# Kernel optimization log

Hardware: AMD Instinct MI355X
Metric: run time of the kernel (lower is better)

Reference implementation:

```python
import jax, jax.numpy as jnp
import numpy as np

D_MODEL = 1024
N_HEAD = 16


def setup_inputs() -> dict:
    key = jax.random.key(0)
    ks = jax.random.split(key, 11)
    B, S, D = 2, 2048, D_MODEL
    scale = 1.0 / np.sqrt(D)
    inp = {
        "q": jax.random.normal(ks[0], (B, S, D), jnp.float32),
        "k": jax.random.normal(ks[1], (B, S, D), jnp.float32),
        "v": jax.random.normal(ks[2], (B, S, D), jnp.float32),
        "w_q": jax.random.normal(ks[3], (D, D), jnp.float32) * scale,
        "b_q": jnp.zeros((D,), jnp.float32),
        "w_k": jax.random.normal(ks[4], (D, D), jnp.float32) * scale,
        "b_k": jnp.zeros((D,), jnp.float32),
        "w_v": jax.random.normal(ks[5], (D, D), jnp.float32) * scale,
        "b_v": jnp.zeros((D,), jnp.float32),
        "w_o": jax.random.normal(ks[6], (D, D), jnp.float32) * scale,
        "b_o": jnp.zeros((D,), jnp.float32),
    }
    return inp


def _split_heads(x, n_head):
    # [B, S, D] -> [B, H, S, Dh]
    B, S, D = x.shape
    return x.reshape(B, S, n_head, D // n_head).transpose(0, 2, 1, 3)


def reference(q, k, v, w_q, b_q, w_k, b_k, w_v, b_v, w_o, b_o):
    # torch Linear: y = x @ W.T + b
    qp = q @ w_q.T + b_q
    kp = k @ w_k.T + b_k
    vp = v @ w_v.T + b_v
    qh = _split_heads(qp, N_HEAD)  # [B,H,S,Dh]
    kh = _split_heads(kp, N_HEAD)
    vh = _split_heads(vp, N_HEAD)
    d_head = qh.shape[-1]
    score = jnp.einsum("bhsd,bhtd->bhst", qh, kh) / jnp.sqrt(jnp.float32(d_head))
    attn = jax.nn.softmax(score, axis=-1)
    out = jnp.einsum("bhst,bhtd->bhsd", attn, vh)  # [B,H,S,Dh]
    B, H, S, Dh = out.shape
    out = out.transpose(0, 2, 1, 3).reshape(B, S, H * Dh)  # concat heads
    return out @ w_o.T + b_o
```

## Files before the change

### kernel.cpp

```cpp
#include <hip/hip_runtime.h>

typedef __bf16 bf16_t;
typedef __bf16 bf16x8 __attribute__((ext_vector_type(8)));
typedef __bf16 bf16x4 __attribute__((ext_vector_type(4)));
typedef float f32x4 __attribute__((ext_vector_type(4)));

#define MFMA16(a, b, c) __builtin_amdgcn_mfma_f32_16x16x32_bf16((a), (b), (c), 0, 0, 0)

#define GLOAD_LDS16(gsrc, ldst)                                                     \
  __builtin_amdgcn_global_load_lds(                                                 \
      (const __attribute__((address_space(1))) void*)(gsrc),                        \
      (__attribute__((address_space(3))) void*)(ldst), 16, 0, 0)

__global__ __launch_bounds__(256) void cast_all(
    const float* __restrict__ s0, const float* __restrict__ s1, const float* __restrict__ s2,
    const float* __restrict__ s3, const float* __restrict__ s4, const float* __restrict__ s5,
    const float* __restrict__ s6,
    bf16_t* __restrict__ d0, bf16_t* __restrict__ d1, bf16_t* __restrict__ d2,
    bf16_t* __restrict__ d3, bf16_t* __restrict__ d4, bf16_t* __restrict__ d5,
    bf16_t* __restrict__ d6) {
  const int a = blockIdx.y;
  const float* s = a == 0 ? s0 : a == 1 ? s1 : a == 2 ? s2 : a == 3 ? s3
                 : a == 4 ? s4 : a == 5 ? s5 : s6;
  bf16_t* d = a == 0 ? d0 : a == 1 ? d1 : a == 2 ? d2 : a == 3 ? d3
            : a == 4 ? d4 : a == 5 ? d5 : d6;
  const int n = a < 3 ? (2 * 2048 * 1024) : (1024 * 1024);
  int i = (blockIdx.x * 256 + threadIdx.x) * 4;
  if (i >= n) return;
  float4 v = *reinterpret_cast<const float4*>(s + i);
  bf16x4 o;
  o[0] = (bf16_t)v.x; o[1] = (bf16_t)v.y; o[2] = (bf16_t)v.z; o[3] = (bf16_t)v.w;
  *reinterpret_cast<bf16x4*>(d + i) = o;
}

template <int OUTF32>
__device__ __forceinline__ void gemm_core(
    const bf16_t* __restrict__ A, const bf16_t* __restrict__ B,
    const float* __restrict__ bias, void* __restrict__ Cout,
    int bm, int bn, float scalep, bf16_t* __restrict__ As, bf16_t* __restrict__ Bs) {
  const int tid = threadIdx.x, lane = tid & 63, wid = tid >> 6;
  const int wr = wid >> 1, wc = wid & 1;
  const int l15 = lane & 15, g = lane >> 4, l7 = l15 & 7;
  const int sr = lane >> 3;
  const int sg = (lane & 7) ^ sr;
  f32x4 acc[4][2] = {};

  const bf16_t* Arow = A + (size_t)(bm + wid * 32 + sr) * 1024 + sg * 8;
  const bf16_t* Brow = B + (size_t)(bn + wid * 16 + sr) * 1024 + sg * 8;

  auto stage = [&](int t, int buf) {
    const int k0 = t * 64;
    bf16_t* Ad = As + buf * 8192 + wid * 2048;
    bf16_t* Bd = Bs + buf * 4096 + wid * 1024;
#pragma unroll
    for (int a = 0; a < 4; a++)
      GLOAD_LDS16(Arow + (size_t)a * 8 * 1024 + k0, Ad + a * 512);
#pragma unroll
    for (int bI = 0; bI < 2; bI++)
      GLOAD_LDS16(Brow + (size_t)bI * 8 * 1024 + k0, Bd + bI * 512);
  };

  stage(0, 0);
  __syncthreads();
  for (int t = 0; t < 16; t++) {
    if (t < 15) stage(t + 1, (t + 1) & 1);
    const bf16_t* Ab = As + (t & 1) * 8192;
    const bf16_t* Bb = Bs + (t & 1) * 4096;
#pragma unroll
    for (int kk = 0; kk < 2; kk++) {
      const int gsw = ((kk * 4 + g) ^ l7) * 8;
      bf16x8 af[4], bfr[2];
#pragma unroll
      for (int mi = 0; mi < 4; mi++)
        af[mi] = *reinterpret_cast<const bf16x8*>(&Ab[(wr * 64 + mi * 16 + l15) * 64 + gsw]);
#pragma unroll
      for (int ni = 0; ni < 2; ni++)
        bfr[ni] = *reinterpret_cast<const bf16x8*>(&Bb[(wc * 32 + ni * 16 + l15) * 64 + gsw]);
      __builtin_amdgcn_s_setprio(1);
#pragma unroll
      for (int mi = 0; mi < 4; mi++)
#pragma unroll
        for (int ni = 0; ni < 2; ni++)
          acc[mi][ni] = MFMA16(af[mi], bfr[ni], acc[mi][ni]);
      __builtin_amdgcn_s_setprio(0);
    }
    __syncthreads();
  }

#pragma unroll
  for (int mi = 0; mi < 4; mi++)
#pragma unroll
    for (int ni = 0; ni < 2; ni++) {
      const int row = bm + wr * 64 + mi * 16 + g * 4;
      const int col = bn + wc * 32 + ni * 16 + l15;
      const float bv = bias[col];
#pragma unroll
      for (int r = 0; r < 4; r++) {
        float v = (acc[mi][ni][r] + bv) * scalep;
        if (OUTF32)
          reinterpret_cast<float*>(Cout)[(size_t)(row + r) * 1024 + col] = v;
        else
          reinterpret_cast<bf16_t*>(Cout)[(size_t)(row + r) * 1024 + col] = (bf16_t)v;
      }
    }
}

__global__ __launch_bounds__(256) void qkv_gemm(
    const bf16_t* __restrict__ qb, const bf16_t* __restrict__ kb, const bf16_t* __restrict__ vb,
    const bf16_t* __restrict__ wqb, const bf16_t* __restrict__ wkb, const bf16_t* __restrict__ wvb,
    const float* __restrict__ bq, const float* __restrict__ bk, const float* __restrict__ bv,
    bf16_t* __restrict__ QP, bf16_t* __restrict__ KP, bf16_t* __restrict__ VP, float qscale) {
  __shared__ bf16_t As[2 * 128 * 64];
  __shared__ bf16_t Bs[2 * 64 * 64];
  const int id = blockIdx.x;
  const int sw = (id & 7) * 192 + (id >> 3);
  const int z = sw >> 9, rem = sw & 511;
  const int by = rem >> 4, bx = rem & 15;
  const bf16_t* A = z == 0 ? qb : z == 1 ? kb : vb;
  const bf16_t* B = z == 0 ? wqb : z == 1 ? wkb : wvb;
  const float* bias = z == 0 ? bq : z == 1 ? bk : bv;
  bf16_t* C = z == 0 ? QP : z == 1 ? KP : VP;
  gemm_core<0>(A, B, bias, C, by * 128, bx * 64, z == 0 ? qscale : 1.0f, As, Bs);
}

__global__ __launch_bounds__(256) void out_gemm(
    const bf16_t* __restrict__ A, const bf16_t* __restrict__ B,
    const float* __restrict__ bias, float* __restrict__ C) {
  __shared__ bf16_t As[2 * 128 * 64];
  __shared__ bf16_t Bs[2 * 64 * 64];
  const int id = blockIdx.x;
  const int sw = (id & 7) * 64 + (id >> 3);
  const int by = sw >> 4, bx = sw & 15;
  gemm_core<1>(A, B, bias, C, by * 128, bx * 64, 1.0f, As, Bs);
}

__global__ __launch_bounds__(256) void transpose_v64(
    const bf16_t* __restrict__ VP, bf16_t* __restrict__ VT) {
  __shared__ bf16_t t[64][72];
  const int tid = threadIdx.x;
  const int bh = blockIdx.y, b = bh >> 4, h = bh & 15;
  const int sbase = blockIdx.x * 64;
#pragma unroll
  for (int i = 0; i < 2; i++) {
    int c = tid + i * 256;
    int r = c >> 3, cc = (c & 7) * 8;
    *reinterpret_cast<bf16x8*>(&t[r][cc]) =
        *reinterpret_cast<const bf16x8*>(&VP[(size_t)(b * 2048 + sbase + r) * 1024 + h * 64 + cc]);
  }
  __syncthreads();
#pragma unroll
  for (int i = 0; i < 2; i++) {
    int c = tid + i * 256;
    int d = c >> 3, scc = (c & 7) * 8;
    bf16x8 v;
#pragma unroll
    for (int j = 0; j < 8; j++) v[j] = t[scc + j][d];
    *reinterpret_cast<bf16x8*>(&VT[(size_t)(bh * 64 + d) * 2048 + sbase + scc]) = v;
  }
}

__global__ __launch_bounds__(512) void attn_fwd(
    const bf16_t* __restrict__ Q, const bf16_t* __restrict__ K,
    const bf16_t* __restrict__ VT, bf16_t* __restrict__ O) {
  __shared__ bf16_t Kl[2 * 64 * 64];
  __shared__ bf16_t Vl[2 * 64 * 64];
  __shared__ bf16_t Pl[8][16 * 64];
  const int tid = threadIdx.x, lane = tid & 63, wid = tid >> 6;
  const int l15 = lane & 15, g = lane >> 4, l7 = l15 & 7;
  const int id = blockIdx.x;
  const int sw = (id & 7) * 64 + (id >> 3);
  const int bh = sw >> 4, qblk = sw & 15;
  const int b = bh >> 4, h = bh & 15;
  const int qbase = qblk * 128;

  const int qrow = b * 2048 + qbase + wid * 16 + l15;
  const bf16x8 qf0 = *reinterpret_cast<const bf16x8*>(&Q[(size_t)qrow * 1024 + h * 64 + g * 8]);
  const bf16x8 qf1 = *reinterpret_cast<const bf16x8*>(&Q[(size_t)qrow * 1024 + h * 64 + 32 + g * 8]);

  const int sr = lane >> 3, sg = (lane & 7) ^ sr;
  const bf16_t* Ksrc = K + (size_t)(b * 2048 + wid * 8 + sr) * 1024 + h * 64 + sg * 8;
  const bf16_t* Vsrc = VT + (size_t)(bh * 64 + wid * 8 + sr) * 2048 + sg * 8;

  float ssum = 0.0f;
  f32x4 oacc[4] = {};

  auto stage = [&](int kt, int buf) {
    GLOAD_LDS16(Ksrc + (size_t)kt * 1024, Kl + buf * 4096 + wid * 512);
    GLOAD_LDS16(Vsrc + kt, Vl + buf * 4096 + wid * 512);
  };

  stage(0, 0);
  __syncthreads();
  for (int t = 0; t < 32; t++) {
    if (t < 31) stage((t + 1) * 64, (t + 1) & 1);
    const bf16_t* Kb = Kl + (t & 1) * 4096;
    const bf16_t* Vb = Vl + (t & 1) * 4096;

    f32x4 sacc[4] = {};
    __builtin_amdgcn_s_setprio(1);
#pragma unroll
    for (int ni = 0; ni < 4; ni++) {
      const int krow = (ni * 16 + l15) * 64;
      bf16x8 kf0 = *reinterpret_cast<const bf16x8*>(&Kb[krow + ((g ^ l7) * 8)]);
      bf16x8 kf1 = *reinterpret_cast<const bf16x8*>(&Kb[krow + (((4 + g) ^ l7) * 8)]);
      sacc[ni] = MFMA16(kf0, qf0, sacc[ni]);
      sacc[ni] = MFMA16(kf1, qf1, sacc[ni]);
    }
    __builtin_amdgcn_s_setprio(0);

    float rs = 0.0f;
#pragma unroll
    for (int ni = 0; ni < 4; ni++)
#pragma unroll
      for (int r = 0; r < 4; r++) {
        float e = exp2f(sacc[ni][r]);
        sacc[ni][r] = e;
        rs += e;
      }
    rs += __shfl_xor(rs, 16);
    rs += __shfl_xor(rs, 32);
    ssum += rs;

#pragma unroll
    for (int ni = 0; ni < 4; ni++) {
      bf16x4 pv;
#pragma unroll
      for (int r = 0; r < 4; r++) pv[r] = (bf16_t)sacc[ni][r];
      *reinterpret_cast<bf16x4*>(
          &Pl[wid][l15 * 64 + (((2 * ni + (g >> 1)) ^ l7) * 8) + (g & 1) * 4]) = pv;
    }

    __builtin_amdgcn_s_setprio(1);
#pragma unroll
    for (int c = 0; c < 2; c++) {
      const int gp = ((c * 4 + g) ^ l7) * 8;
      bf16x8 pf = *reinterpret_cast<const bf16x8*>(&Pl[wid][l15 * 64 + gp]);
#pragma unroll
      for (int dn = 0; dn < 4; dn++) {
        bf16x8 vf = *reinterpret_cast<const bf16x8*>(&Vb[(dn * 16 + l15) * 64 + gp]);
        oacc[dn] = MFMA16(pf, vf, oacc[dn]);
      }
    }
    __builtin_amdgcn_s_setprio(0);
    __syncthreads();
  }

  float si[4];
#pragma unroll
  for (int r = 0; r < 4; r++) si[r] = 1.0f / __shfl(ssum, g * 4 + r);
  const int orow = b * 2048 + qbase + wid * 16 + g * 4;
#pragma unroll
  for (int dn = 0; dn < 4; dn++)
#pragma unroll
    for (int r = 0; r < 4; r++)
      O[(size_t)(orow + r) * 1024 + h * 64 + dn * 16 + l15] = (bf16_t)(oacc[dn][r] * si[r]);
}

extern "C" void kernel_launch(void* const* d_in, const int* in_sizes, int n_in,
                              void* d_out, int out_size, void* d_ws, size_t ws_size,
                              hipStream_t stream) {
  const float* q  = (const float*)d_in[0];
  const float* k  = (const float*)d_in[1];
  const float* v  = (const float*)d_in[2];
  const float* wq = (const float*)d_in[3];
  const float* bq = (const float*)d_in[4];
  const float* wk = (const float*)d_in[5];
  const float* bk = (const float*)d_in[6];
  const float* wv = (const float*)d_in[7];
  const float* bv = (const float*)d_in[8];
  const float* wo = (const float*)d_in[9];
  const float* bo = (const float*)d_in[10];

  char* ws = (char*)d_ws;
  const size_t MB = 1024 * 1024;
  bf16_t* qb  = (bf16_t*)(ws + 0 * MB);
  bf16_t* kb  = (bf16_t*)(ws + 8 * MB);
  bf16_t* vb  = (bf16_t*)(ws + 16 * MB);
  bf16_t* QP  = (bf16_t*)(ws + 24 * MB);
  bf16_t* KP  = (bf16_t*)(ws + 32 * MB);
  bf16_t* VP  = (bf16_t*)(ws + 40 * MB);
  bf16_t* wqb = (bf16_t*)(ws + 48 * MB);
  bf16_t* wkb = (bf16_t*)(ws + 50 * MB);
  bf16_t* wvb = (bf16_t*)(ws + 52 * MB);
  bf16_t* wob = (bf16_t*)(ws + 54 * MB);
  bf16_t* VTb = (bf16_t*)(ws + 8 * MB);
  bf16_t* AO  = (bf16_t*)(ws + 0 * MB);

  const float QSCALE = 0.125f * 1.44269504089f;

  cast_all<<<dim3(4096, 7), 256, 0, stream>>>(q, k, v, wq, wk, wv, wo,
                                              qb, kb, vb, wqb, wkb, wvb, wob);
  qkv_gemm<<<1536, 256, 0, stream>>>(qb, kb, vb, wqb, wkb, wvb, bq, bk, bv,
                                     QP, KP, VP, QSCALE);
  transpose_v64<<<dim3(32, 32), 256, 0, stream>>>(VP, VTb);
  attn_fwd<<<512, 512, 0, stream>>>(QP, KP, VTb, AO);
  out_gemm<<<512, 256, 0, stream>>>(AO, wob, bo, (float*)d_out);
}
```

Baseline: 237.8 us.

## Triple-buffer GEMM K-loop with explicit vmcnt waits, retile QKV, shrink attention blocks

```diff
diff --git a/kernel.cpp b/kernel.cpp
--- a/kernel.cpp
+++ b/kernel.cpp
@@ -33,66 +33,73 @@
   *reinterpret_cast<bf16x4*>(d + i) = o;
 }
 
-template <int OUTF32>
-__device__ __forceinline__ void gemm_core(
+template <int OUTF32, int NFRAG>
+__device__ __forceinline__ void gemm_core3(
     const bf16_t* __restrict__ A, const bf16_t* __restrict__ B,
     const float* __restrict__ bias, void* __restrict__ Cout,
     int bm, int bn, float scalep, bf16_t* __restrict__ As, bf16_t* __restrict__ Bs) {
   const int tid = threadIdx.x, lane = tid & 63, wid = tid >> 6;
   const int wr = wid >> 1, wc = wid & 1;
-  const int l15 = lane & 15, g = lane >> 4, l7 = l15 & 7;
-  const int sr = lane >> 3;
-  const int sg = (lane & 7) ^ sr;
-  f32x4 acc[4][2] = {};
-
-  const bf16_t* Arow = A + (size_t)(bm + wid * 32 + sr) * 1024 + sg * 8;
-  const bf16_t* Brow = B + (size_t)(bn + wid * 16 + sr) * 1024 + sg * 8;
-
-  auto stage = [&](int t, int buf) {
-    const int k0 = t * 64;
-    bf16_t* Ad = As + buf * 8192 + wid * 2048;
-    bf16_t* Bd = Bs + buf * 4096 + wid * 1024;
-#pragma unroll
-    for (int a = 0; a < 4; a++)
-      GLOAD_LDS16(Arow + (size_t)a * 8 * 1024 + k0, Ad + a * 512);
-#pragma unroll
-    for (int bI = 0; bI < 2; bI++)
-      GLOAD_LDS16(Brow + (size_t)bI * 8 * 1024 + k0, Bd + bI * 512);
+  const int l15 = lane & 15, g = lane >> 4;
+  f32x4 acc[4][NFRAG] = {};
+
+  constexpr int ABUF = 4096;
+  constexpr int BBUF = NFRAG * 1024;
+
+  const int arow = wid * 16 + (lane >> 2);
+  const int sc = (lane & 3) * 8;
+  const bf16_t* Ap0 = A + (size_t)(bm + arow) * 1024 + sc;
+  const bf16_t* Ap1 = Ap0 + (size_t)64 * 1024;
+  const bf16_t* Bp0 = B + (size_t)(bn + arow) * 1024 + sc;
+  const bf16_t* Bp1 = Bp0 + (size_t)64 * 1024;
+
+  auto stage = [&](int k0, int buf) {
+    bf16_t* Ad = As + buf * ABUF;
+    bf16_t* Bd = Bs + buf * BBUF;
+    GLOAD_LDS16(Ap0 + k0, Ad + wid * 512);
+    GLOAD_LDS16(Ap1 + k0, Ad + 2048 + wid * 512);
+    GLOAD_LDS16(Bp0 + k0, Bd + wid * 512);
+    if constexpr (NFRAG == 4) GLOAD_LDS16(Bp1 + k0, Bd + 2048 + wid * 512);
   };
 
   stage(0, 0);
-  __syncthreads();
-  for (int t = 0; t < 16; t++) {
-    if (t < 15) stage(t + 1, (t + 1) & 1);
-    const bf16_t* Ab = As + (t & 1) * 8192;
-    const bf16_t* Bb = Bs + (t & 1) * 4096;
-#pragma unroll
-    for (int kk = 0; kk < 2; kk++) {
-      const int gsw = ((kk * 4 + g) ^ l7) * 8;
-      bf16x8 af[4], bfr[2];
-#pragma unroll
-      for (int mi = 0; mi < 4; mi++)
-        af[mi] = *reinterpret_cast<const bf16x8*>(&Ab[(wr * 64 + mi * 16 + l15) * 64 + gsw]);
-#pragma unroll
-      for (int ni = 0; ni < 2; ni++)
-        bfr[ni] = *reinterpret_cast<const bf16x8*>(&Bb[(wc * 32 + ni * 16 + l15) * 64 + gsw]);
-      __builtin_amdgcn_s_setprio(1);
-#pragma unroll
-      for (int mi = 0; mi < 4; mi++)
-#pragma unroll
-        for (int ni = 0; ni < 2; ni++)
-          acc[mi][ni] = MFMA16(af[mi], bfr[ni], acc[mi][ni]);
-      __builtin_amdgcn_s_setprio(0);
-    }
-    __syncthreads();
+  stage(32, 1);
+  for (int t = 0; t < 32; t++) {
+    const int kn = (t < 30) ? (t + 2) * 32 : 0;
+    stage(kn, (t + 2) % 3);
+    if constexpr (NFRAG == 4)
+      asm volatile("s_waitcnt vmcnt(8)" ::: "memory");
+    else
+      asm volatile("s_waitcnt vmcnt(6)" ::: "memory");
+    __builtin_amdgcn_s_barrier();
+    __builtin_amdgcn_sched_barrier(0);
+    const bf16_t* Ab = As + (t % 3) * ABUF;
+    const bf16_t* Bb = Bs + (t % 3) * BBUF;
+    bf16x8 af[4], bfr[NFRAG];
+#pragma unroll
+    for (int mi = 0; mi < 4; mi++)
+      af[mi] = *reinterpret_cast<const bf16x8*>(&Ab[(wr * 64 + mi * 16 + l15) * 32 + g * 8]);
+#pragma unroll
+    for (int ni = 0; ni < NFRAG; ni++)
+      bfr[ni] = *reinterpret_cast<const bf16x8*>(
+          &Bb[(wc * (NFRAG * 16) + ni * 16 + l15) * 32 + g * 8]);
+    __builtin_amdgcn_s_setprio(1);
+#pragma unroll
+    for (int mi = 0; mi < 4; mi++)
+#pragma unroll
+      for (int ni = 0; ni < NFRAG; ni++)
+        acc[mi][ni] = MFMA16(af[mi], bfr[ni], acc[mi][ni]);
+    __builtin_amdgcn_s_setprio(0);
+    __builtin_amdgcn_sched_barrier(0);
+    __builtin_amdgcn_s_barrier();
   }
 
 #pragma unroll
   for (int mi = 0; mi < 4; mi++)
 #pragma unroll
-    for (int ni = 0; ni < 2; ni++) {
+    for (int ni = 0; ni < NFRAG; ni++) {
       const int row = bm + wr * 64 + mi * 16 + g * 4;
-      const int col = bn + wc * 32 + ni * 16 + l15;
+      const int col = bn + wc * (NFRAG * 16) + ni * 16 + l15;
       const float bv = bias[col];
 #pragma unroll
       for (int r = 0; r < 4; r++) {
@@ -110,28 +117,28 @@
     const bf16_t* __restrict__ wqb, const bf16_t* __restrict__ wkb, const bf16_t* __restrict__ wvb,
     const float* __restrict__ bq, const float* __restrict__ bk, const float* __restrict__ bv,
     bf16_t* __restrict__ QP, bf16_t* __restrict__ KP, bf16_t* __restrict__ VP, float qscale) {
-  __shared__ bf16_t As[2 * 128 * 64];
-  __shared__ bf16_t Bs[2 * 64 * 64];
+  __shared__ bf16_t As[3 * 4096];
+  __shared__ bf16_t Bs[3 * 4096];
   const int id = blockIdx.x;
-  const int sw = (id & 7) * 192 + (id >> 3);
-  const int z = sw >> 9, rem = sw & 511;
-  const int by = rem >> 4, bx = rem & 15;
+  const int sw = (id & 7) * 96 + (id >> 3);
+  const int z = sw >> 8, rem = sw & 255;
+  const int by = rem >> 3, bx = rem & 7;
   const bf16_t* A = z == 0 ? qb : z == 1 ? kb : vb;
   const bf16_t* B = z == 0 ? wqb : z == 1 ? wkb : wvb;
   const float* bias = z == 0 ? bq : z == 1 ? bk : bv;
   bf16_t* C = z == 0 ? QP : z == 1 ? KP : VP;
-  gemm_core<0>(A, B, bias, C, by * 128, bx * 64, z == 0 ? qscale : 1.0f, As, Bs);
+  gemm_core3<0, 4>(A, B, bias, C, by * 128, bx * 128, z == 0 ? qscale : 1.0f, As, Bs);
 }
 
 __global__ __launch_bounds__(256) void out_gemm(
     const bf16_t* __restrict__ A, const bf16_t* __restrict__ B,
     const float* __restrict__ bias, float* __restrict__ C) {
-  __shared__ bf16_t As[2 * 128 * 64];
-  __shared__ bf16_t Bs[2 * 64 * 64];
+  __shared__ bf16_t As[3 * 4096];
+  __shared__ bf16_t Bs[3 * 2048];
   const int id = blockIdx.x;
   const int sw = (id & 7) * 64 + (id >> 3);
   const int by = sw >> 4, bx = sw & 15;
-  gemm_core<1>(A, B, bias, C, by * 128, bx * 64, 1.0f, As, Bs);
+  gemm_core3<1, 2>(A, B, bias, C, by * 128, bx * 64, 1.0f, As, Bs);
 }
 
 __global__ __launch_bounds__(256) void transpose_v64(
@@ -159,40 +166,48 @@
   }
 }
 
-__global__ __launch_bounds__(512) void attn_fwd(
+__global__ __launch_bounds__(256) void attn_fwd(
     const bf16_t* __restrict__ Q, const bf16_t* __restrict__ K,
     const bf16_t* __restrict__ VT, bf16_t* __restrict__ O) {
-  __shared__ bf16_t Kl[2 * 64 * 64];
-  __shared__ bf16_t Vl[2 * 64 * 64];
-  __shared__ bf16_t Pl[8][16 * 64];
+  __shared__ bf16_t Kl[2 * 4096];
+  __shared__ bf16_t Vl[2 * 4096];
+  __shared__ bf16_t Pl[4][1024];
   const int tid = threadIdx.x, lane = tid & 63, wid = tid >> 6;
   const int l15 = lane & 15, g = lane >> 4, l7 = l15 & 7;
   const int id = blockIdx.x;
-  const int sw = (id & 7) * 64 + (id >> 3);
-  const int bh = sw >> 4, qblk = sw & 15;
+  const int sw = (id & 7) * 128 + (id >> 3);
+  const int bh = sw >> 5, qblk = sw & 31;
   const int b = bh >> 4, h = bh & 15;
-  const int qbase = qblk * 128;
+  const int qbase = qblk * 64;
 
   const int qrow = b * 2048 + qbase + wid * 16 + l15;
   const bf16x8 qf0 = *reinterpret_cast<const bf16x8*>(&Q[(size_t)qrow * 1024 + h * 64 + g * 8]);
   const bf16x8 qf1 = *reinterpret_cast<const bf16x8*>(&Q[(size_t)qrow * 1024 + h * 64 + 32 + g * 8]);
 
-  const int sr = lane >> 3, sg = (lane & 7) ^ sr;
-  const bf16_t* Ksrc = K + (size_t)(b * 2048 + wid * 8 + sr) * 1024 + h * 64 + sg * 8;
-  const bf16_t* Vsrc = VT + (size_t)(bh * 64 + wid * 8 + sr) * 2048 + sg * 8;
+  const int srow = lane >> 3;
+  const int sg = (lane & 7) ^ srow;
+  const bf16_t* Ksrc = K + (size_t)(b * 2048 + wid * 16 + srow) * 1024 + h * 64 + sg * 8;
+  const bf16_t* Vsrc = VT + (size_t)(bh * 64 + wid * 16 + srow) * 2048 + sg * 8;
+
+  auto stage = [&](int kt, int buf) {
+    bf16_t* Kd = Kl + buf * 4096 + wid * 1024;
+    bf16_t* Vd = Vl + buf * 4096 + wid * 1024;
+    GLOAD_LDS16(Ksrc + (size_t)kt * 1024, Kd);
+    GLOAD_LDS16(Ksrc + (size_t)(kt + 8) * 1024, Kd + 512);
+    GLOAD_LDS16(Vsrc + kt, Vd);
+    GLOAD_LDS16(Vsrc + kt + 8 * 2048, Vd + 512);
+  };
 
   float ssum = 0.0f;
   f32x4 oacc[4] = {};
 
-  auto stage = [&](int kt, int buf) {
-    GLOAD_LDS16(Ksrc + (size_t)kt * 1024, Kl + buf * 4096 + wid * 512);
-    GLOAD_LDS16(Vsrc + kt, Vl + buf * 4096 + wid * 512);
-  };
-
   stage(0, 0);
-  __syncthreads();
   for (int t = 0; t < 32; t++) {
-    if (t < 31) stage((t + 1) * 64, (t + 1) & 1);
+    const int ktn = (t < 31) ? (t + 1) * 64 : 0;
+    stage(ktn, (t + 1) & 1);
+    asm volatile("s_waitcnt vmcnt(4)" ::: "memory");
+    __builtin_amdgcn_s_barrier();
+    __builtin_amdgcn_sched_barrier(0);
     const bf16_t* Kb = Kl + (t & 1) * 4096;
     const bf16_t* Vb = Vl + (t & 1) * 4096;
 
@@ -242,7 +257,8 @@
       }
     }
     __builtin_amdgcn_s_setprio(0);
-    __syncthreads();
+    __builtin_amdgcn_sched_barrier(0);
+    __builtin_amdgcn_s_barrier();
   }
 
   float si[4];
@@ -290,9 +306,9 @@
 
   cast_all<<<dim3(4096, 7), 256, 0, stream>>>(q, k, v, wq, wk, wv, wo,
                                               qb, kb, vb, wqb, wkb, wvb, wob);
-  qkv_gemm<<<1536, 256, 0, stream>>>(qb, kb, vb, wqb, wkb, wvb, bq, bk, bv,
-                                     QP, KP, VP, QSCALE);
+  qkv_gemm<<<768, 256, 0, stream>>>(qb, kb, vb, wqb, wkb, wvb, bq, bk, bv,
+                                    QP, KP, VP, QSCALE);
   transpose_v64<<<dim3(32, 32), 256, 0, stream>>>(VP, VTb);
-  attn_fwd<<<512, 512, 0, stream>>>(QP, KP, VTb, AO);
+  attn_fwd<<<1024, 256, 0, stream>>>(QP, KP, VTb, AO);
   out_gemm<<<512, 256, 0, stream>>>(AO, wob, bo, (float*)d_out);
 }
```

Result: slower. 247.1 us (+3.9%).
